# Optimization experiments

Hardware: AMD Instinct MI355X
Metric: run time of the kernel (lower is better)

Reference implementation:

```python
import jax, jax.numpy as jnp
import numpy as np

N_Q = 16384; N_S = 16384; NN = 32; F_IN = 128; F_OUT = 256
K = 15; DIM = 3
RADIUS = 10.0
KP_EXTENT_CFG = 1.0      # config.NETWORK.KP_EXTENT (also scales learned offsets)
DENSITY = 5.0            # config.NETWORK.DENSITY_PARAMETER
EXTENT = KP_EXTENT_CFG * RADIUS / DENSITY   # 2.0
K_RADIUS = 1.5 * EXTENT
OFFSET_DIM = DIM * (K - 1)  # modulated=False, version=0 -> 42


def setup_inputs() -> dict:
    key = jax.random.key(0)
    ks = jax.random.split(key, 8)
    query_points = jax.random.uniform(ks[0], (N_Q, DIM), dtype=jnp.float32)
    support_points = jax.random.uniform(ks[1], (N_S, DIM), dtype=jnp.float32)
    neighbors = jax.random.randint(ks[2], (N_Q, NN), 0, N_S)
    features = jax.random.normal(ks[3], (N_S, F_IN), dtype=jnp.float32)
    # kernel points: fixed disposition inside ball of radius 1.5*extent, first point at center
    kp = jax.random.normal(ks[4], (K, DIM), dtype=jnp.float32)
    kp = kp / jnp.linalg.norm(kp, axis=1, keepdims=True) * (0.7 * K_RADIUS)
    K_points = kp.at[0].set(0.0)
    weight = jax.random.normal(ks[5], (K, F_IN, F_OUT), dtype=jnp.float32) / np.sqrt(F_IN)
    deformable_weight = jax.random.normal(ks[6], (K, F_IN, OFFSET_DIM), dtype=jnp.float32) / np.sqrt(F_IN)
    bias = jnp.zeros((OFFSET_DIM,), dtype=jnp.float32)
    return {"query_points": query_points, "support_points": support_points,
            "neighbors": neighbors, "features": features, "K_points": K_points,
            "weight": weight, "deformable_weight": deformable_weight, "bias": bias}


def _gather_neighb(query_points, support_points, neighbors, features):
    # pad with shadow point (far away) and zero feature row, as in KPConv_ops
    sp = jnp.concatenate([support_points, jnp.full((1, DIM), 1e6, support_points.dtype)], 0)
    ft = jnp.concatenate([features, jnp.zeros((1, features.shape[1]), features.dtype)], 0)
    rel = sp[neighbors] - query_points[:, None, :]   # [n, nn, 3]
    nfeat = ft[neighbors]                            # [n, nn, f]
    return rel, nfeat


def _linear_influence(sq_dist):
    # KP_INFLUENCE='linear': relu(1 - d/extent); CONVOLUTION_MODE='sum'
    return jnp.maximum(1.0 - jnp.sqrt(sq_dist) / EXTENT, 0.0)


def reference(query_points, support_points, neighbors, features, K_points,
              weight, deformable_weight, bias):
    rel, nfeat = _gather_neighb(query_points, support_points, neighbors, features)

    # --- rigid KPConv producing offsets (version=0) ---
    d0 = rel[:, :, None, :] - K_points[None, None, :, :]   # [n, nn, K, 3]
    sq0 = jnp.sum(d0 * d0, axis=-1)                        # [n, nn, K]
    w0 = _linear_influence(sq0)
    wf0 = jnp.einsum('enk,enf->ekf', w0, nfeat)            # [n, K, f]
    feat0 = jnp.einsum('ekf,kfo->eo', wf0, deformable_weight) + bias  # [n, 42]

    # not modulated: reshape to offsets, prepend zero offset for center kernel point
    offsets = feat0.reshape(-1, K - 1, DIM)
    offsets = jnp.concatenate([jnp.zeros_like(offsets[:, :1, :]), offsets], axis=1)
    offsets = offsets * KP_EXTENT_CFG                      # [n, K, 3]

    # --- deformable KPConv ---
    def_kp = K_points[None, :, :] + offsets                # [n, K, 3]
    d1 = rel[:, :, None, :] - def_kp[:, None, :, :]        # [n, nn, K, 3]
    sq1 = jnp.sum(d1 * d1, axis=-1)                        # [n, nn, K]
    w1 = _linear_influence(sq1)                            # out-of-range neighbors get 0 weight
    wf1 = jnp.einsum('enk,enf->ekf', w1, nfeat)            # [n, K, f]
    out = jnp.einsum('ekf,kfo->eo', wf1, weight)           # [n, f_out]
    return out
```

## Files before the change

### kernel.cpp

```cpp
#include <hip/hip_runtime.h>
#include <hip/hip_bf16.h>
#include <math.h>

typedef __attribute__((ext_vector_type(8))) short bf16x8;
typedef __attribute__((ext_vector_type(4))) float f32x4;

#define NQ 16384
#define NN 32
#define FI 128
#define FO 256
#define KPN 15
#define OD 42
#define INV_EXT 0.5f

#define WS_FP1    0u
#define WS_FP2    (8u * 1024u * 1024u)
#define WS_BSW    (12u * 1024u * 1024u)
#define WS_DWBH   (13u * 1024u * 1024u)
#define WS_DWBL   (WS_DWBH + 196608u)
#define WS_DEFKP  (14u * 1024u * 1024u)

static __device__ __forceinline__ unsigned short f2bf(float x) {
    union { __hip_bfloat16 h; unsigned short u; } cv;
    cv.h = __float2bfloat16(x);
    return cv.u;
}
static __device__ __forceinline__ float bf2f(unsigned short h) {
    union { unsigned int u; float f; } cv;
    cv.u = ((unsigned int)h) << 16;
    return cv.f;
}

union U8 { unsigned short u[8]; bf16x8 v; };

__global__ void pre_all(const float* __restrict__ feat,
                        unsigned int* __restrict__ fp1, unsigned int* __restrict__ fp2,
                        const float* __restrict__ w, unsigned short* __restrict__ Bsw,
                        const float* __restrict__ dw,
                        unsigned short* __restrict__ dhi, unsigned short* __restrict__ dlo)
{
    const int b = blockIdx.x, t = threadIdx.x;
    if (b < 1024) {
        const int g  = b * 256 + t;
        const int lq = g & 3;
        const int fp = (g >> 2) & 3;
        const int s  = g >> 4;
        const float4* f4 = (const float4*)feat;
        const float4 A = f4[s * 32 + fp * 8 + lq];
        const float4 C = f4[s * 32 + fp * 8 + 4 + lq];
        const float av[4] = {A.x, A.y, A.z, A.w};
        const float cv[4] = {C.x, C.y, C.z, C.w};
        unsigned int pw[8];
        #pragma unroll
        for (int e = 0; e < 4; e++) {
            const unsigned short ha = f2bf(av[e]), hc = f2bf(cv[e]);
            const unsigned short la = f2bf(av[e] - bf2f(ha));
            const unsigned short lc = f2bf(cv[e] - bf2f(hc));
            pw[2 * e]     = (unsigned int)ha | ((unsigned int)hc << 16);
            pw[2 * e + 1] = (unsigned int)la | ((unsigned int)lc << 16);
            fp2[s * 64 + (fp >> 1) * 32 + (lq * 4 + e) * 2 + (fp & 1)] =
                (unsigned int)ha | ((unsigned int)hc << 16);
        }
        *(uint4*)&fp1[s * 128 + fp * 32 + lq * 8]     = *(uint4*)&pw[0];
        *(uint4*)&fp1[s * 128 + fp * 32 + lq * 8 + 4] = *(uint4*)&pw[4];
    } else if (b < 1024 + 256) {
        const int tid = (b - 1024) * 256 + t;
        const int lane = tid & 63;
        const int kt   = (tid >> 6) & 63;
        const int nt   = tid >> 12;
        const int n    = nt * 16 + (lane & 15);
        const int kbase = kt * 32 + (lane >> 4) * 8;
        unsigned int p[4];
        #pragma unroll
        for (int jj = 0; jj < 4; jj++) {
            unsigned int lo, hi;
            {
                const int kk = kbase + 2 * jj;
                const int f = kk >> 4, k = kk & 15;
                lo = (k < KPN) ? f2bf(w[(k * FI + f) * FO + n]) : 0u;
            }
            {
                const int kk = kbase + 2 * jj + 1;
                const int f = kk >> 4, k = kk & 15;
                hi = (k < KPN) ? f2bf(w[(k * FI + f) * FO + n]) : 0u;
            }
            p[jj] = lo | (hi << 16);
        }
        unsigned int* op = (unsigned int*)&Bsw[tid * 8];
        op[0] = p[0]; op[1] = p[1]; op[2] = p[2]; op[3] = p[3];
    } else {
        const int tid = (b - 1280) * 256 + t;
        const int lane = tid & 63;
        const int kt   = (tid >> 6) & 63;
        const int nt   = tid >> 12;
        const int o    = nt * 16 + (lane & 15);
        const int kbase = kt * 32 + (lane >> 4) * 8;
        #pragma unroll
        for (int j = 0; j < 8; j++) {
            const int kf = kbase + j;
            const int f = kf >> 4, k = kf & 15;
            float v = (k < KPN && o < OD) ? dw[(k * FI + f) * OD + o] : 0.f;
            unsigned short h = f2bf(v);
            dhi[tid * 8 + j] = h;
            dlo[tid * 8 + j] = f2bf(v - bf2f(h));
        }
    }
}

__global__ __launch_bounds__(512, 4)
void k1_offsets(const float* __restrict__ query, const float* __restrict__ support,
                const int* __restrict__ neighbors, const unsigned int* __restrict__ fp1,
                const float* __restrict__ kpoints,
                const unsigned short* __restrict__ dwB_hi,
                const unsigned short* __restrict__ dwB_lo,
                const float* __restrict__ bias, float* __restrict__ defkp)
{
    __shared__ unsigned short wf_hi[8192];
    __shared__ unsigned short wf_lo[8192];
    __shared__ float relx[512], rely[512], relz[512];
    __shared__ int   nbr_s[512];
    __shared__ float kp_s[48];
    __shared__ f32x4 cred[3 * 64];

    const int t = threadIdx.x;
    const int qbase = blockIdx.x * 16;
    if (t < 45) kp_s[t] = kpoints[t];
    if (t >= 45 && t < 48) kp_s[t] = 0.f;

    {
        const int e = t >> 5, n = t & 31;
        const int q = qbase + e;
        const int idx = neighbors[q * NN + n];
        nbr_s[t] = idx;
        relx[t] = support[idx * 3 + 0] - query[q * 3 + 0];
        rely[t] = support[idx * 3 + 1] - query[q * 3 + 1];
        relz[t] = support[idx * 3 + 2] - query[q * 3 + 2];
    }
    __syncthreads();

    const int wave = t >> 6, lane = t & 63;
    const int quad = lane >> 4, low = lane & 15;
    const int kb = (low < KPN) ? low * 3 : 0;

    U8 ah[2], al[2];
    {
        const float kx = kp_s[kb + 0], ky = kp_s[kb + 1], kz = kp_s[kb + 2];
        #pragma unroll
        for (int ei = 0; ei < 2; ei++) {
            const int ee = wave * 2 + ei;
            #pragma unroll
            for (int j = 0; j < 8; j++) {
                const int ni = ee * 32 + quad * 8 + j;
                const float dx = relx[ni] - kx;
                const float dy = rely[ni] - ky;
                const float dz = relz[ni] - kz;
                const float d = sqrtf(dx * dx + dy * dy + dz * dz);
                float w = 1.0f - d * INV_EXT;
                w = (low < KPN && w > 0.f) ? w : 0.f;
                const unsigned short h = f2bf(w);
                ah[ei].u[j] = h;
                al[ei].u[j] = f2bf(w - bf2f(h));
            }
        }
    }

    f32x4 acc = {0.f, 0.f, 0.f, 0.f};
    const int nt = wave >> 1, half = wave & 1;
    const uint2* fp1v = (const uint2*)fp1;
    const bf16x8* Bh = (const bf16x8*)dwB_hi;
    const bf16x8* Bl = (const bf16x8*)dwB_lo;

    for (int c = 0; c < 4; c++) {
        #pragma unroll
        for (int ei = 0; ei < 2; ei++) {
            const int ee = wave * 2 + ei;
            union { unsigned int u[4]; bf16x8 v; } bhA, blA, bhB, blB;
            #pragma unroll
            for (int jj = 0; jj < 4; jj++) {
                const int r0 = nbr_s[ee * 32 + quad * 8 + 2 * jj];
                const int r1 = nbr_s[ee * 32 + quad * 8 + 2 * jj + 1];
                const uint2 d0 = fp1v[r0 * 64 + c * 16 + low];
                const uint2 d1 = fp1v[r1 * 64 + c * 16 + low];
                bhA.u[jj] = __builtin_amdgcn_perm(d1.x, d0.x, 0x05040100u);
                bhB.u[jj] = __builtin_amdgcn_perm(d1.x, d0.x, 0x07060302u);
                blA.u[jj] = __builtin_amdgcn_perm(d1.y, d0.y, 0x05040100u);
                blB.u[jj] = __builtin_amdgcn_perm(d1.y, d0.y, 0x07060302u);
            }
            #pragma unroll
            for (int hh2 = 0; hh2 < 2; hh2++) {
                const bf16x8 bh = hh2 ? bhB.v : bhA.v;
                const bf16x8 bl = hh2 ? blB.v : blA.v;
                f32x4 o = {0.f, 0.f, 0.f, 0.f};
                o = __builtin_amdgcn_mfma_f32_16x16x32_bf16(al[ei].v, bh, o, 0, 0, 0);
                o = __builtin_amdgcn_mfma_f32_16x16x32_bf16(ah[ei].v, bl, o, 0, 0, 0);
                o = __builtin_amdgcn_mfma_f32_16x16x32_bf16(ah[ei].v, bh, o, 0, 0, 0);
                const int fc   = hh2 * 16 + low;
                const int cblk = fc + (quad >> 1) * 32;
                const int slot = ee ^ (fc & 15);
                const int hw   = cblk * 128 + slot * 8 + (quad & 1) * 4;
                const unsigned short h0 = f2bf(o[0]), h1 = f2bf(o[1]);
                const unsigned short h2 = f2bf(o[2]), h3 = f2bf(o[3]);
                uint2 ph;
                ph.x = (unsigned int)h0 | ((unsigned int)h1 << 16);
                ph.y = (unsigned int)h2 | ((unsigned int)h3 << 16);
                *(uint2*)&wf_hi[hw] = ph;
                uint2 pl;
                pl.x = (unsigned int)f2bf(o[0] - bf2f(h0)) |
                       ((unsigned int)f2bf(o[1] - bf2f(h1)) << 16);
                pl.y = (unsigned int)f2bf(o[2] - bf2f(h2)) |
                       ((unsigned int)f2bf(o[3] - bf2f(h3)) << 16);
                *(uint2*)&wf_lo[hw] = pl;
            }
        }
        __syncthreads();
        if (wave < 6) {
            #pragma unroll 4
            for (int ktl = half * 8; ktl < half * 8 + 8; ktl++) {
                const int fc   = ktl * 2 + (quad >> 1);
                const int cblk = fc + (quad & 1) * 32;
                const int slot = low ^ (fc & 15);
                const int hw   = cblk * 128 + slot * 8;
                bf16x8 a_h = *(const bf16x8*)&wf_hi[hw];
                bf16x8 a_l = *(const bf16x8*)&wf_lo[hw];
                const int ktg = c * 16 + ktl;
                bf16x8 b_h = Bh[(nt * 64 + ktg) * 64 + lane];
                bf16x8 b_l = Bl[(nt * 64 + ktg) * 64 + lane];
                acc = __builtin_amdgcn_mfma_f32_16x16x32_bf16(a_l, b_h, acc, 0, 0, 0);
                acc = __builtin_amdgcn_mfma_f32_16x16x32_bf16(a_h, b_l, acc, 0, 0, 0);
                acc = __builtin_amdgcn_mfma_f32_16x16x32_bf16(a_h, b_h, acc, 0, 0, 0);
            }
        } else if (c == 0 && wave == 6 && lane < 48) {
            defkp[(qbase + lane / 3) * 45 + (lane % 3)] = kp_s[lane % 3];
        }
        __syncthreads();
    }

    if (wave < 6 && half == 1) cred[nt * 64 + lane] = acc;
    __syncthreads();
    if (wave < 6 && half == 0) {
        f32x4 o2 = cred[nt * 64 + lane];
        acc[0] += o2[0]; acc[1] += o2[1]; acc[2] += o2[2]; acc[3] += o2[3];
        const int o = nt * 16 + low;
        if (o < OD) {
            const float bo = bias[o] + kp_s[3 + o];
            #pragma unroll
            for (int r = 0; r < 4; r++) {
                const int ee = quad * 4 + r;
                defkp[(qbase + ee) * 45 + 3 + o] = bo + acc[r];
            }
        }
    }
}

__global__ __launch_bounds__(512, 4)
void k2_deform(const float* __restrict__ query, const float* __restrict__ support,
               const int* __restrict__ neighbors, const unsigned int* __restrict__ fp2,
               const unsigned short* __restrict__ Bsw, const float* __restrict__ defkp,
               float* __restrict__ out)
{
    __shared__ unsigned short wf2[32768];
    __shared__ unsigned short nbr_s[1024];

    float* relx = (float*)wf2;
    float* rely = relx + 1024;
    float* relz = relx + 2048;
    float* dk_s = relx + 3072;

    const int t = threadIdx.x;
    const int qbase = blockIdx.x * 32;

    for (int i = t; i < 32 * 45; i += 512) dk_s[i] = defkp[qbase * 45 + i];
    #pragma unroll
    for (int ii = 0; ii < 2; ii++) {
        const int i = ii * 512 + t;
        const int e = i >> 5, n = i & 31;
        const int q = qbase + e;
        const int idx = neighbors[q * NN + n];
        nbr_s[i] = (unsigned short)idx;
        relx[i] = support[idx * 3 + 0] - query[q * 3 + 0];
        rely[i] = support[idx * 3 + 1] - query[q * 3 + 1];
        relz[i] = support[idx * 3 + 2] - query[q * 3 + 2];
    }
    __syncthreads();

    const int wave = t >> 6, lane = t & 63;
    const int quad = lane >> 4, low = lane & 15;
    const int kb = (low < KPN) ? low * 3 : 0;

    U8 af[4];
    #pragma unroll
    for (int ei = 0; ei < 4; ei++) {
        const int ee = wave * 4 + ei;
        const float kx = dk_s[ee * 45 + kb + 0];
        const float ky = dk_s[ee * 45 + kb + 1];
        const float kz = dk_s[ee * 45 + kb + 2];
        #pragma unroll
        for (int j = 0; j < 8; j++) {
            const int ni = ee * 32 + quad * 8 + j;
            const float dx = relx[ni] - kx;
            const float dy = rely[ni] - ky;
            const float dz = relz[ni] - kz;
            const float d = sqrtf(dx * dx + dy * dy + dz * dz);
            float w = 1.0f - d * INV_EXT;
            w = (low < KPN && w > 0.f) ? w : 0.f;
            af[ei].u[j] = f2bf(w);
        }
    }
    __syncthreads();

    f32x4 acc00 = {0,0,0,0}, acc01 = {0,0,0,0};
    f32x4 acc10 = {0,0,0,0}, acc11 = {0,0,0,0};
    const int nt0 = wave * 2, nt1 = nt0 + 1;
    const bf16x8* Bp = (const bf16x8*)Bsw;
    const uint2* fp2v = (const uint2*)fp2;

    for (int c2 = 0; c2 < 2; c2++) {
        #pragma unroll
        for (int ei = 0; ei < 4; ei++) {
            const int ee = wave * 4 + ei;
            union { unsigned int u[4]; bf16x8 v; } b00, b01, b10, b11;
            #pragma unroll
            for (int jj = 0; jj < 4; jj++) {
                const int r0 = nbr_s[ee * 32 + quad * 8 + 2 * jj];
                const int r1 = nbr_s[ee * 32 + quad * 8 + 2 * jj + 1];
                const uint2 g0 = fp2v[r0 * 32 + c2 * 16 + low];
                const uint2 g1 = fp2v[r1 * 32 + c2 * 16 + low];
                b00.u[jj] = __builtin_amdgcn_perm(g1.x, g0.x, 0x05040100u);
                b01.u[jj] = __builtin_amdgcn_perm(g1.x, g0.x, 0x07060302u);
                b10.u[jj] = __builtin_amdgcn_perm(g1.y, g0.y, 0x05040100u);
                b11.u[jj] = __builtin_amdgcn_perm(g1.y, g0.y, 0x07060302u);
            }
            #pragma unroll
            for (int p = 0; p < 2; p++) {
                #pragma unroll
                for (int hh2 = 0; hh2 < 2; hh2++) {
                    const bf16x8 b = p ? (hh2 ? b11.v : b10.v)
                                       : (hh2 ? b01.v : b00.v);
                    f32x4 o = {0.f, 0.f, 0.f, 0.f};
                    o = __builtin_amdgcn_mfma_f32_16x16x32_bf16(af[ei].v, b, o, 0, 0, 0);
                    const int fc   = hh2 * 16 + low;
                    const int cblk = fc + (quad >> 1) * 32;
                    const int slot = ee ^ fc;
                    const int hw   = p * 16384 + cblk * 256 + slot * 8 + (quad & 1) * 4;
                    uint2 ph;
                    ph.x = (unsigned int)f2bf(o[0]) | ((unsigned int)f2bf(o[1]) << 16);
                    ph.y = (unsigned int)f2bf(o[2]) | ((unsigned int)f2bf(o[3]) << 16);
                    *(uint2*)&wf2[hw] = ph;
                }
            }
        }
        __syncthreads();
        #pragma unroll
        for (int p = 0; p < 2; p++) {
            #pragma unroll 4
            for (int ktl = 0; ktl < 16; ktl++) {
                const int fc   = ktl * 2 + (quad >> 1);
                const int cblk = fc + (quad & 1) * 32;
                const int s0 = (low ^ fc) * 8;
                const int s1 = ((16 + low) ^ fc) * 8;
                bf16x8 a0 = *(const bf16x8*)&wf2[p * 16384 + cblk * 256 + s0];
                bf16x8 a1 = *(const bf16x8*)&wf2[p * 16384 + cblk * 256 + s1];
                const int ktg = (2 * c2 + p) * 16 + ktl;
                bf16x8 b0 = Bp[(nt0 * 64 + ktg) * 64 + lane];
                bf16x8 b1 = Bp[(nt1 * 64 + ktg) * 64 + lane];
                acc00 = __builtin_amdgcn_mfma_f32_16x16x32_bf16(a0, b0, acc00, 0, 0, 0);
                acc01 = __builtin_amdgcn_mfma_f32_16x16x32_bf16(a0, b1, acc01, 0, 0, 0);
                acc10 = __builtin_amdgcn_mfma_f32_16x16x32_bf16(a1, b0, acc10, 0, 0, 0);
                acc11 = __builtin_amdgcn_mfma_f32_16x16x32_bf16(a1, b1, acc11, 0, 0, 0);
            }
        }
        __syncthreads();
    }

    #pragma unroll
    for (int r = 0; r < 4; r++) {
        const int e0 = quad * 4 + r;
        out[(qbase + e0) * FO + nt0 * 16 + low] = acc00[r];
        out[(qbase + e0) * FO + nt1 * 16 + low] = acc01[r];
        out[(qbase + 16 + e0) * FO + nt0 * 16 + low] = acc10[r];
        out[(qbase + 16 + e0) * FO + nt1 * 16 + low] = acc11[r];
    }
}

extern "C" void kernel_launch(void* const* d_in, const int* in_sizes, int n_in,
                              void* d_out, int out_size, void* d_ws, size_t ws_size,
                              hipStream_t stream) {
    const float* query     = (const float*)d_in[0];
    const float* support   = (const float*)d_in[1];
    const int*   neighbors = (const int*)  d_in[2];
    const float* features  = (const float*)d_in[3];
    const float* kpoints   = (const float*)d_in[4];
    const float* weight    = (const float*)d_in[5];
    const float* dweight   = (const float*)d_in[6];
    const float* bias      = (const float*)d_in[7];
    float*       out       = (float*)d_out;

    char* ws = (char*)d_ws;
    unsigned int*   fp1  = (unsigned int*)(ws + WS_FP1);
    unsigned int*   fp2  = (unsigned int*)(ws + WS_FP2);
    unsigned short* Bsw  = (unsigned short*)(ws + WS_BSW);
    unsigned short* dwBh = (unsigned short*)(ws + WS_DWBH);
    unsigned short* dwBl = (unsigned short*)(ws + WS_DWBL);
    float*          defkp = (float*)(ws + WS_DEFKP);

    pre_all<<<1328, 256, 0, stream>>>(features, fp1, fp2, weight, Bsw,
                                      dweight, dwBh, dwBl);
    k1_offsets<<<NQ / 16, 512, 0, stream>>>(query, support, neighbors, fp1,
                                            kpoints, dwBh, dwBl, bias, defkp);
    k2_deform<<<NQ / 32, 512, 0, stream>>>(query, support, neighbors, fp2,
                                           Bsw, defkp, out);
}
```

Before: 165.2 us.

## Double-buffer k1 weighted-feature tiles and prefetch next chunk gathers

The offset kernel now keeps two LDS buffers for the weighted-feature tiles. It issues the global gathers for chunk c+1 before the matmul on chunk c, then builds the next tile after it, which removes one barrier per iteration. The aim is to hide gather latency behind MFMA work. In exchange, LDS use doubles and register pressure grows from the 16 prefetched uint2 values, which could cut occupancy under launch_bounds(512,4).

Result: slower. 172.4 us (+4.3%).

```diff
diff --git a/kernel.cpp b/kernel.cpp
--- a/kernel.cpp
+++ b/kernel.cpp
@@ -115,8 +115,8 @@
                 const unsigned short* __restrict__ dwB_lo,
                 const float* __restrict__ bias, float* __restrict__ defkp)
 {
-    __shared__ unsigned short wf_hi[8192];
-    __shared__ unsigned short wf_lo[8192];
+    __shared__ unsigned short wf_hi[2][8192];
+    __shared__ unsigned short wf_lo[2][8192];
     __shared__ float relx[512], rely[512], relz[512];
     __shared__ int   nbr_s[512];
     __shared__ float kp_s[48];
@@ -170,49 +170,68 @@
     const bf16x8* Bh = (const bf16x8*)dwB_hi;
     const bf16x8* Bl = (const bf16x8*)dwB_lo;
 
+    uint2 g[2][4][2];
+
+#define K1_ISSUE(CC)                                                          \
+    _Pragma("unroll")                                                         \
+    for (int ei = 0; ei < 2; ei++) {                                          \
+        const int ee = wave * 2 + ei;                                         \
+        _Pragma("unroll")                                                     \
+        for (int jj = 0; jj < 4; jj++) {                                      \
+            const int r0 = nbr_s[ee * 32 + quad * 8 + 2 * jj];                \
+            const int r1 = nbr_s[ee * 32 + quad * 8 + 2 * jj + 1];            \
+            g[ei][jj][0] = fp1v[r0 * 64 + (CC) * 16 + low];                   \
+            g[ei][jj][1] = fp1v[r1 * 64 + (CC) * 16 + low];                   \
+        }                                                                     \
+    }
+
+#define K1_BUILD(CC)                                                          \
+    _Pragma("unroll")                                                         \
+    for (int ei = 0; ei < 2; ei++) {                                          \
+        const int ee = wave * 2 + ei;                                         \
+        union { unsigned int u[4]; bf16x8 v; } bhA, blA, bhB, blB;            \
+        _Pragma("unroll")                                                     \
+        for (int jj = 0; jj < 4; jj++) {                                      \
+            const uint2 d0 = g[ei][jj][0];                                    \
+            const uint2 d1 = g[ei][jj][1];                                    \
+            bhA.u[jj] = __builtin_amdgcn_perm(d1.x, d0.x, 0x05040100u);       \
+            bhB.u[jj] = __builtin_amdgcn_perm(d1.x, d0.x, 0x07060302u);       \
+            blA.u[jj] = __builtin_amdgcn_perm(d1.y, d0.y, 0x05040100u);       \
+            blB.u[jj] = __builtin_amdgcn_perm(d1.y, d0.y, 0x07060302u);       \
+        }                                                                     \
+        _Pragma("unroll")                                                     \
+        for (int hh2 = 0; hh2 < 2; hh2++) {                                   \
+            const bf16x8 bh = hh2 ? bhB.v : bhA.v;                            \
+            const bf16x8 bl = hh2 ? blB.v : blA.v;                            \
+            f32x4 o = {0.f, 0.f, 0.f, 0.f};                                   \
+            o = __builtin_amdgcn_mfma_f32_16x16x32_bf16(al[ei].v, bh, o, 0, 0, 0); \
+            o = __builtin_amdgcn_mfma_f32_16x16x32_bf16(ah[ei].v, bl, o, 0, 0, 0); \
+            o = __builtin_amdgcn_mfma_f32_16x16x32_bf16(ah[ei].v, bh, o, 0, 0, 0); \
+            const int fc   = hh2 * 16 + low;                                  \
+            const int cblk = fc + (quad >> 1) * 32;                           \
+            const int slot = ee ^ (fc & 15);                                  \
+            const int hw   = cblk * 128 + slot * 8 + (quad & 1) * 4;          \
+            const unsigned short h0 = f2bf(o[0]), h1 = f2bf(o[1]);            \
+            const unsigned short h2 = f2bf(o[2]), h3 = f2bf(o[3]);            \
+            uint2 ph;                                                         \
+            ph.x = (unsigned int)h0 | ((unsigned int)h1 << 16);               \
+            ph.y = (unsigned int)h2 | ((unsigned int)h3 << 16);               \
+            *(uint2*)&wf_hi[(CC) & 1][hw] = ph;                               \
+            uint2 pl;                                                         \
+            pl.x = (unsigned int)f2bf(o[0] - bf2f(h0)) |                      \
+                   ((unsigned int)f2bf(o[1] - bf2f(h1)) << 16);               \
+            pl.y = (unsigned int)f2bf(o[2] - bf2f(h2)) |                      \
+                   ((unsigned int)f2bf(o[3] - bf2f(h3)) << 16);               \
+            *(uint2*)&wf_lo[(CC) & 1][hw] = pl;                               \
+        }                                                                     \
+    }
+
+    K1_ISSUE(0)
+    K1_BUILD(0)
+    __syncthreads();
+
     for (int c = 0; c < 4; c++) {
-        #pragma unroll
-        for (int ei = 0; ei < 2; ei++) {
-            const int ee = wave * 2 + ei;
-            union { unsigned int u[4]; bf16x8 v; } bhA, blA, bhB, blB;
-            #pragma unroll
-            for (int jj = 0; jj < 4; jj++) {
-                const int r0 = nbr_s[ee * 32 + quad * 8 + 2 * jj];
-                const int r1 = nbr_s[ee * 32 + quad * 8 + 2 * jj + 1];
-                const uint2 d0 = fp1v[r0 * 64 + c * 16 + low];
-                const uint2 d1 = fp1v[r1 * 64 + c * 16 + low];
-                bhA.u[jj] = __builtin_amdgcn_perm(d1.x, d0.x, 0x05040100u);
-                bhB.u[jj] = __builtin_amdgcn_perm(d1.x, d0.x, 0x07060302u);
-                blA.u[jj] = __builtin_amdgcn_perm(d1.y, d0.y, 0x05040100u);
-                blB.u[jj] = __builtin_amdgcn_perm(d1.y, d0.y, 0x07060302u);
-            }
-            #pragma unroll
-            for (int hh2 = 0; hh2 < 2; hh2++) {
-                const bf16x8 bh = hh2 ? bhB.v : bhA.v;
-                const bf16x8 bl = hh2 ? blB.v : blA.v;
-                f32x4 o = {0.f, 0.f, 0.f, 0.f};
-                o = __builtin_amdgcn_mfma_f32_16x16x32_bf16(al[ei].v, bh, o, 0, 0, 0);
-                o = __builtin_amdgcn_mfma_f32_16x16x32_bf16(ah[ei].v, bl, o, 0, 0, 0);
-                o = __builtin_amdgcn_mfma_f32_16x16x32_bf16(ah[ei].v, bh, o, 0, 0, 0);
-                const int fc   = hh2 * 16 + low;
-                const int cblk = fc + (quad >> 1) * 32;
-                const int slot = ee ^ (fc & 15);
-                const int hw   = cblk * 128 + slot * 8 + (quad & 1) * 4;
-                const unsigned short h0 = f2bf(o[0]), h1 = f2bf(o[1]);
-                const unsigned short h2 = f2bf(o[2]), h3 = f2bf(o[3]);
-                uint2 ph;
-                ph.x = (unsigned int)h0 | ((unsigned int)h1 << 16);
-                ph.y = (unsigned int)h2 | ((unsigned int)h3 << 16);
-                *(uint2*)&wf_hi[hw] = ph;
-                uint2 pl;
-                pl.x = (unsigned int)f2bf(o[0] - bf2f(h0)) |
-                       ((unsigned int)f2bf(o[1] - bf2f(h1)) << 16);
-                pl.y = (unsigned int)f2bf(o[2] - bf2f(h2)) |
-                       ((unsigned int)f2bf(o[3] - bf2f(h3)) << 16);
-                *(uint2*)&wf_lo[hw] = pl;
-            }
-        }
-        __syncthreads();
+        if (c < 3) { K1_ISSUE(c + 1) }
         if (wave < 6) {
             #pragma unroll 4
             for (int ktl = half * 8; ktl < half * 8 + 8; ktl++) {
@@ -220,8 +239,8 @@
                 const int cblk = fc + (quad & 1) * 32;
                 const int slot = low ^ (fc & 15);
                 const int hw   = cblk * 128 + slot * 8;
-                bf16x8 a_h = *(const bf16x8*)&wf_hi[hw];
-                bf16x8 a_l = *(const bf16x8*)&wf_lo[hw];
+                bf16x8 a_h = *(const bf16x8*)&wf_hi[c & 1][hw];
+                bf16x8 a_l = *(const bf16x8*)&wf_lo[c & 1][hw];
                 const int ktg = c * 16 + ktl;
                 bf16x8 b_h = Bh[(nt * 64 + ktg) * 64 + lane];
                 bf16x8 b_l = Bl[(nt * 64 + ktg) * 64 + lane];
@@ -232,6 +251,7 @@
         } else if (c == 0 && wave == 6 && lane < 48) {
             defkp[(qbase + lane / 3) * 45 + (lane % 3)] = kp_s[lane % 3];
         }
+        if (c < 3) { K1_BUILD(c + 1) }
         __syncthreads();
     }
 
@@ -250,6 +270,8 @@
             }
         }
     }
+#undef K1_ISSUE
+#undef K1_BUILD
 }
 
 __global__ __launch_bounds__(512, 4)
```
